# Kernel tuning notes

Hardware: AMD Instinct MI355X
Metric: run time of the kernel (lower is better)

Reference implementation:

```python
import jax, jax.numpy as jnp
import numpy as np

_CODESZ = 8
_INT_MAP = (2 ** np.arange(_CODESZ))[::-1].astype(np.int32)  # [128,64,...,1], MSB = dim 0

_NORM12 = np.array([
    [3,1,1,1,3,3,3,3],[1,3,1,1,3,3,3,3],[1,1,3,1,3,3,3,3],[1,1,1,3,3,3,3,3],
    [3,3,3,1,3,3,1,1],[3,3,3,1,3,1,3,1],[3,3,3,1,1,3,3,1],[3,3,3,1,3,1,1,3],
    [3,3,3,1,1,3,1,3],[3,3,3,1,1,1,3,3],[3,3,1,3,3,3,1,1],[3,3,1,3,3,1,3,1],
    [3,3,1,3,1,3,3,1],[3,3,1,3,3,1,1,3],[3,3,1,3,1,3,1,3],[3,3,1,3,1,1,3,3],
    [3,1,3,3,3,3,1,1],[3,1,3,3,3,1,3,1],[3,1,3,3,1,3,3,1],[3,1,3,3,3,1,1,3],
    [3,1,3,3,1,3,1,3],[1,3,3,3,1,1,3,3],[1,3,3,3,3,3,1,1],[1,3,3,3,3,1,3,1],
    [1,3,3,3,1,3,3,1],[1,3,3,3,3,1,1,3],[1,3,3,3,1,3,1,3],[1,3,3,3,1,1,3,3],
    [3,3,1,1,3,3,3,1]], dtype=np.float32) / 2.0


def _build_codebook():
    # abs grid: nonneg half-integer vectors with norm^2 <= 10 == abs of even-sum D8+1/2 shell
    vals = np.array([0.5, 1.5, 2.5], np.float32)  # 3.5^2 > 10, so components <= 2.5
    pts = np.stack(np.meshgrid(*([vals] * _CODESZ), indexing='ij'), -1).reshape(-1, _CODESZ)
    pts = pts[(pts * pts).sum(-1) <= 10.0]                      # 227 rows
    pts = pts[np.lexsort(pts[:, ::-1].T)]                       # torch.unique(dim=0) order
    absg = np.concatenate([pts, _NORM12], 0)                    # [256, 8]

    bits = ((np.arange(256)[:, None] & _INT_MAP[None, :]) > 0).astype(np.int32)  # [256,8]
    pop = bits.sum(-1)
    even_ids = np.where(pop % 2 == 0)[0]                        # 128 even-parity masks
    odd_ids = np.where(pop % 2 == 1)[0]
    signs_even = (1 - 2 * bits[even_ids]).astype(np.float32)    # [128,8]
    signs_odd = (1 - 2 * bits[odd_ids]).astype(np.float32)
    # valid sign parity per abs entry so flipped point has even coordinate sum
    g_even = (absg.sum(-1) % 2.0) == 0.0
    S = np.where(g_even[:, None, None], signs_even[None], signs_odd[None])  # [256,128,8]
    P = (S * absg[:, None, :]).reshape(-1, _CODESZ)             # [32768,8] shell points
    # full grid = [P + 1/4 ; P - 1/4]  (grid[:half] - 1/4 == P, as the module assumes)

    # grid_part: canonical representatives (dims 1: have <=1 negative, min >= -0.5)
    sel = ((P[:, 1:] < 0).sum(-1) <= 1) & (P[:, 1:].min(-1) >= -0.5)
    grid_part = P[sel]                                          # [G,8]
    grid_part_norm = (grid_part * grid_part).sum(-1)            # [G]

    # iterate_mask: even-parity flips x grid_part -> index into grid
    flips = (1 - 2 * bits[even_ids]).astype(np.float32)         # [128,8]
    idx_map = np.zeros(256, np.int32)
    idx_map[even_ids] = np.arange(128, dtype=np.int32)
    gridH = P + 0.25                                            # first half of grid
    gridHn = (gridH * gridH).sum(-1)
    allcombo_idx = np.zeros((128, len(grid_part)), np.int32)
    for i in range(128):  # small fixed loop over sign masks, as in the original
        sc = 2.0 * ((flips[i] * grid_part) @ gridH.T) - gridHn
        allcombo_idx[i] = np.argmax(sc, -1).astype(np.int32)
    # _E8P_GRID_IDX taken as identity permutation -> grid_idx_map = arange - 2^15 (int16)
    grid_idx_map = (np.arange(2 ** 16) - 2 ** 15).astype(np.int16)
    return grid_part, grid_part_norm, allcombo_idx, idx_map, grid_idx_map


def setup_inputs() -> dict:
    key = jax.random.key(0)
    N = 131072
    grid_part, gpn, aci, imap, gim = _build_codebook()
    X = jax.random.normal(key, (N, _CODESZ), dtype=jnp.float32)
    return {
        'X': X,
        'grid_part': jnp.asarray(grid_part),
        'grid_part_norm': jnp.asarray(gpn),
        'allcombo_idx': jnp.asarray(aci),
        'idx_map': jnp.asarray(imap),
        'int_map': jnp.asarray(_INT_MAP),
        'grid_idx_map': jnp.asarray(gim),
    }


def reference(X, grid_part, grid_part_norm, allcombo_idx, idx_map, int_map, grid_idx_map):
    def fast_quantize_part(Y):
        neg = Y < 0                                              # [N,8]
        odd = (neg.sum(-1) % 2) == 1                             # [N] odd # of negatives
        Ya = jnp.abs(Y)
        Ya = Ya.at[:, 0].set(jnp.where(odd, -Ya[:, 0], Ya[:, 0]))
        mask = jnp.where(neg, -1.0, 1.0).astype(Y.dtype)
        mask = mask.at[:, 0].set(jnp.where(odd, -mask[:, 0], mask[:, 0]))
        # nearest codeword: argmax(2 Y.g - |g|^2)  == argmin |Y - g|^2
        q = jnp.argmax(2.0 * (Ya @ grid_part.T) - grid_part_norm, axis=-1)  # [N]
        vals = grid_part[q] * mask
        mint = (((1.0 - mask) * 0.5).astype(jnp.int32) * int_map).sum(-1)   # bit-pack signs
        real_idx = allcombo_idx[idx_map[mint], q]
        err = jnp.sqrt(((Y - vals) ** 2).sum(-1))
        return vals, real_idx, err

    HALF = 2 ** 15
    pv, pi, pe = fast_quantize_part(X + 0.25)
    mv, mi, me = fast_quantize_part(X - 0.25)
    which = pe < me
    final_vals = jnp.where(which[:, None], pv - 0.25, mv + 0.25)
    final_idxs = grid_idx_map[jnp.where(which, pi + HALF, mi)]
    return final_vals, final_idxs
```

## Files before the change

### kernel.cpp

```cpp
#include <hip/hip_runtime.h>
#include <hip/hip_bf16.h>

typedef __attribute__((ext_vector_type(8)))  short bf16x8;
typedef __attribute__((ext_vector_type(16))) float f32x16;

#define TPB 256
#define SCORE_MARGIN 1e-3f
#define ERR_MARGIN   1e-3f

static __device__ __forceinline__ unsigned short bf16_rne(float v) {
    union { __hip_bfloat16 h; unsigned short u; } cv;
    cv.h = __float2bfloat16(v);
    return cv.u;
}
static __device__ __forceinline__ float bfhi(unsigned u) { return __uint_as_float(u << 16); }
static __device__ __forceinline__ float bflo(unsigned u) { return __uint_as_float(u & 0xffff0000u); }

__global__ __launch_bounds__(TPB, 4) void e8p_fused(
    const float* __restrict__ X,
    const float* __restrict__ grid_part,
    const float* __restrict__ grid_part_norm,
    const int*   __restrict__ allcombo_idx,
    const int*   __restrict__ idx_map,
    float* __restrict__ out,
    int N, int G, int T)
{
    extern __shared__ __align__(16) unsigned char smem[];
    const int T32 = T * 32;
    unsigned char* ldsG = smem;
    unsigned short* ldsN = (unsigned short*)(smem + (size_t)T32 * 16);

    const int tid = threadIdx.x;

    for (int c = tid; c < T32; c += TPB) {
        uint4 gv; float nv;
        if (c < G) {
            const float4 g0 = *(const float4*)(grid_part + (size_t)c * 8);
            const float4 g1 = *(const float4*)(grid_part + (size_t)c * 8 + 4);
            gv.x = (unsigned)bf16_rne(g0.x) | ((unsigned)bf16_rne(g0.y) << 16);
            gv.y = (unsigned)bf16_rne(g0.z) | ((unsigned)bf16_rne(g0.w) << 16);
            gv.z = (unsigned)bf16_rne(g1.x) | ((unsigned)bf16_rne(g1.y) << 16);
            gv.w = (unsigned)bf16_rne(g1.z) | ((unsigned)bf16_rne(g1.w) << 16);
            nv = -0.5f * grid_part_norm[c];
        } else {
            gv.x = gv.y = gv.z = gv.w = 0u;
            nv = -30000.0f;
        }
        *(uint4*)(ldsG + (size_t)c * 16) = gv;
        const int t = c >> 5, w = c & 31;
        const int hh = (w >> 2) & 1;
        const int rr = (w & 3) + 4 * (w >> 3);
        ldsN[t * 32 + hh * 16 + rr] = bf16_rne(nv);
    }
    __syncthreads();

    const int lane = tid & 63;
    const int h    = lane >> 5;
    const int col  = lane & 31;
    const int wave = blockIdx.x * (TPB / 64) + (tid >> 6);

    const int li     = col >> 1;
    const int branch = col & 1;
    const int irow   = wave * 16 + li;
    const int iload  = (irow < N) ? irow : 0;

    float x[8];
    {
        const float4 a = *(const float4*)(X + (size_t)iload * 8);
        const float4 b = *(const float4*)(X + (size_t)iload * 8 + 4);
        x[0]=a.x; x[1]=a.y; x[2]=a.z; x[3]=a.w;
        x[4]=b.x; x[5]=b.y; x[6]=b.z; x[7]=b.w;
    }

    float ya[8]; int neg = 0;
    const float sh = branch ? -0.25f : 0.25f;
#pragma unroll
    for (int j = 0; j < 8; ++j) {
        const float yj = x[j] + sh;
        if (yj < 0.0f) neg |= (1 << (7 - j));
        ya[j] = fabsf(yj);
    }
    int mint = neg;
    if (__popc(neg) & 1) { ya[0] = -ya[0]; mint ^= 128; }

    bf16x8 bfrag;
#pragma unroll
    for (int j = 0; j < 8; ++j) {
        const unsigned short hi = bf16_rne(ya[j]);
        const unsigned short lo = bf16_rne(ya[j] - bfhi((unsigned)hi));
        bfrag[j] = (short)(h ? lo : hi);
    }

    float best[4], sec[4]; int qt[4];
#pragma unroll
    for (int g = 0; g < 4; ++g) { best[g] = -1e30f; sec[g] = -1e30f; qt[g] = 0; }

    const unsigned aoff = (unsigned)col * 16u;
    const unsigned char* nbase = (const unsigned char*)ldsN + h * 32;

    bf16x8 afragN = *(const bf16x8*)(ldsG + aoff);
    uint4 n0N = *(const uint4*)(nbase);
    uint4 n1N = *(const uint4*)(nbase + 16);

    for (int t = 0; t < T; ++t) {
        const bf16x8 afrag = afragN;
        const uint4 n0 = n0N, n1 = n1N;
        const int tn = (t + 1 < T) ? (t + 1) : t;
        afragN = *(const bf16x8*)(ldsG + (size_t)tn * 512 + aoff);
        n0N = *(const uint4*)(nbase + (size_t)tn * 64);
        n1N = *(const uint4*)(nbase + (size_t)tn * 64 + 16);

        f32x16 acc;
        acc[0]=bfhi(n0.x);  acc[1]=bflo(n0.x);  acc[2]=bfhi(n0.y);  acc[3]=bflo(n0.y);
        acc[4]=bfhi(n0.z);  acc[5]=bflo(n0.z);  acc[6]=bfhi(n0.w);  acc[7]=bflo(n0.w);
        acc[8]=bfhi(n1.x);  acc[9]=bflo(n1.x);  acc[10]=bfhi(n1.y); acc[11]=bflo(n1.y);
        acc[12]=bfhi(n1.z); acc[13]=bflo(n1.z); acc[14]=bfhi(n1.w); acc[15]=bflo(n1.w);
        acc = __builtin_amdgcn_mfma_f32_32x32x16_bf16(afrag, bfrag, acc, 0, 0, 0);

#pragma unroll
        for (int g = 0; g < 4; ++g) {
            const float m = fmaxf(fmaxf(acc[4*g], acc[4*g+1]),
                                  fmaxf(acc[4*g+2], acc[4*g+3]));
            const bool gt = m > best[g];
            sec[g]  = __builtin_amdgcn_fmed3f(m, best[g], sec[g]);
            best[g] = fmaxf(best[g], m);
            qt[g]   = gt ? t : qt[g];
        }
    }

    float bb = best[0], ss = sec[0];
    int   ib = (qt[0] << 5) + 4 * h;
#pragma unroll
    for (int g = 1; g < 4; ++g) {
        const int ibg = (qt[g] << 5) + 8 * g + 4 * h;
        const float br = best[g];
        ss = fmaxf(fmaxf(ss, sec[g]), fminf(bb, br));
        const bool take = (br > bb) || ((br == bb) && (ibg < ib));
        bb = fmaxf(bb, br);
        ib = take ? ibg : ib;
    }
    {
        const float ob = __shfl_xor(bb, 32, 64);
        const float os = __shfl_xor(ss, 32, 64);
        const int   oi = __shfl_xor(ib, 32, 64);
        ss = fmaxf(fmaxf(ss, os), fminf(bb, ob));
        const bool take = (ob > bb) || ((ob == bb) && (oi < ib));
        bb = fmaxf(bb, ob);
        ib = take ? oi : ib;
    }

    float hiF[8], loF[8];
#pragma unroll
    for (int j = 0; j < 8; ++j) {
        hiF[j] = bfhi((unsigned)bf16_rne(ya[j]));
        loF[j] = ya[j] - hiF[j];
    }
    const int tW   = ib >> 5;
    const int base = ib & 31;
    float sm = -1e30f, sec4 = -1e30f; int km = 0;
#pragma unroll
    for (int k = 0; k < 4; ++k) {
        const int w  = base + k;
        const uint4 gv = *(const uint4*)(ldsG + ((size_t)tW * 32 + w) * 16);
        const int hn = (w >> 2) & 1;
        const int rn = (w & 3) + 4 * (w >> 3);
        const float nv = bfhi((unsigned)ldsN[tW * 32 + hn * 16 + rn]);
        float g0 = bfhi(gv.x), g1 = bflo(gv.x), g2 = bfhi(gv.y), g3 = bflo(gv.y);
        float g4 = bfhi(gv.z), g5 = bflo(gv.z), g6 = bfhi(gv.w), g7 = bflo(gv.w);
        float s = nv;
        s = fmaf(hiF[0], g0, s); s = fmaf(hiF[1], g1, s);
        s = fmaf(hiF[2], g2, s); s = fmaf(hiF[3], g3, s);
        s = fmaf(hiF[4], g4, s); s = fmaf(hiF[5], g5, s);
        s = fmaf(hiF[6], g6, s); s = fmaf(hiF[7], g7, s);
        s = fmaf(loF[0], g0, s); s = fmaf(loF[1], g1, s);
        s = fmaf(loF[2], g2, s); s = fmaf(loF[3], g3, s);
        s = fmaf(loF[4], g4, s); s = fmaf(loF[5], g5, s);
        s = fmaf(loF[6], g6, s); s = fmaf(loF[7], g7, s);
        const bool gt = s > sm;
        sec4 = __builtin_amdgcn_fmed3f(s, sm, sec4);
        sm   = fmaxf(sm, s);
        km   = gt ? k : km;
    }
    const int  qfin   = tW * 32 + base + km;
    const int  closeB = ((sm - sec4) < SCORE_MARGIN) | ((bb - ss) < SCORE_MARGIN);

    const int qO     = __shfl_xor(qfin, 1, 64);
    const int closeO = __shfl_xor(closeB, 1, 64);
    const int mintO  = __shfl_xor(mint, 1, 64);

    const bool doEpi = (h == 0) && (branch == 0) && (irow < N);
    bool close = false;
    if (doEpi) {
        const int qP = qfin, qM = qO;
        const float* gp_ = grid_part + (size_t)qP * 8;
        const float* gm_ = grid_part + (size_t)qM * 8;
        float vp[8], vm[8];
        float ep2 = 0.0f, em2 = 0.0f;
        bool coin = true;
#pragma unroll
        for (int j = 0; j < 8; ++j) {
            const float maskp = ((mint  >> (7 - j)) & 1) ? -1.0f : 1.0f;
            const float maskm = ((mintO >> (7 - j)) & 1) ? -1.0f : 1.0f;
            vp[j] = gp_[j] * maskp;
            vm[j] = gm_[j] * maskm;
            coin = coin && ((vp[j] - 0.25f) == (vm[j] + 0.25f));
            const float dpj = (x[j] + 0.25f) - vp[j];
            const float dmj = (x[j] - 0.25f) - vm[j];
            ep2 = fmaf(dpj, dpj, ep2);
            em2 = fmaf(dmj, dmj, em2);
        }
        close = closeB | closeO | (!coin && (fabsf(ep2 - em2) < ERR_MARGIN));
        if (!close) {
            const bool which = coin ? false : (ep2 < em2);
            const int rowp = idx_map[mint];
            const int rowm = idx_map[mintO];
            const int pi = allcombo_idx[(size_t)rowp * G + qP];
            const int mi = allcombo_idx[(size_t)rowm * G + qM];
            const float idxval = which ? (float)pi : (float)(mi - 32768);
            float* vout = out + (size_t)irow * 8;
#pragma unroll
            for (int j = 0; j < 8; ++j)
                vout[j] = which ? (vp[j] - 0.25f) : (vm[j] + 0.25f);
            out[(size_t)N * 8 + irow] = idxval;
        }
    }

    unsigned long long mb = __ballot(doEpi && close);
    while (mb) {
        const int b = (int)__ffsll(mb) - 1;
        mb &= (mb - 1);
        const int liF = b >> 1;
        const int iF  = wave * 16 + liF;
        float xf[8];
#pragma unroll
        for (int j = 0; j < 8; ++j) xf[j] = __shfl(x[j], b, 64);

        double yapF[8], yamF[8];
        int negp = 0, negm = 0;
#pragma unroll
        for (int j = 0; j < 8; ++j) {
            const double xd = (double)xf[j];
            const double ypd = xd + 0.25;
            const double ymd = xd - 0.25;
            if (ypd < 0.0) negp |= (1 << (7 - j));
            if (ymd < 0.0) negm |= (1 << (7 - j));
            yapF[j] = fabs(ypd);
            yamF[j] = fabs(ymd);
        }
        int mintpF = negp, mintmF = negm;
        if (__popc(negp) & 1) { yapF[0] = -yapF[0]; mintpF ^= 128; }
        if (__popc(negm) & 1) { yamF[0] = -yamF[0]; mintmF ^= 128; }

        double bestpF = -1e300, bestmF = -1e300;
        int qpF = 0x7fffffff, qmF = 0x7fffffff;
        for (int j = lane; j < G; j += 64) {
            const float4 g0 = *(const float4*)(grid_part + (size_t)j * 8);
            const float4 g1 = *(const float4*)(grid_part + (size_t)j * 8 + 4);
            const double n = (double)grid_part_norm[j];
            const double t0 = (double)g0.x, t1 = (double)g0.y,
                         t2 = (double)g0.z, t3 = (double)g0.w,
                         t4 = (double)g1.x, t5 = (double)g1.y,
                         t6 = (double)g1.z, t7 = (double)g1.w;
            double dp, dm;
            dp = yapF[0] * t0;           dm = yamF[0] * t0;
            dp = fma(yapF[1], t1, dp);   dm = fma(yamF[1], t1, dm);
            dp = fma(yapF[2], t2, dp);   dm = fma(yamF[2], t2, dm);
            dp = fma(yapF[3], t3, dp);   dm = fma(yamF[3], t3, dm);
            dp = fma(yapF[4], t4, dp);   dm = fma(yamF[4], t4, dm);
            dp = fma(yapF[5], t5, dp);   dm = fma(yamF[5], t5, dm);
            dp = fma(yapF[6], t6, dp);   dm = fma(yamF[6], t6, dm);
            dp = fma(yapF[7], t7, dp);   dm = fma(yamF[7], t7, dm);
            const double sp = 2.0 * dp - n;
            const double sm2 = 2.0 * dm - n;
            if (sp > bestpF) { bestpF = sp; qpF = j; }
            if (sm2 > bestmF) { bestmF = sm2; qmF = j; }
        }
#pragma unroll
        for (int off = 32; off > 0; off >>= 1) {
            double ob = __shfl_xor(bestpF, off, 64);
            int    oq = __shfl_xor(qpF, off, 64);
            if (ob > bestpF || (ob == bestpF && oq < qpF)) { bestpF = ob; qpF = oq; }
            ob = __shfl_xor(bestmF, off, 64);
            oq = __shfl_xor(qmF, off, 64);
            if (ob > bestmF || (ob == bestmF && oq < qmF)) { bestmF = ob; qmF = oq; }
        }
        if (lane == 0) {
            const float* gp_ = grid_part + (size_t)qpF * 8;
            const float* gm_ = grid_part + (size_t)qmF * 8;
            double vp[8], vm[8];
            double ep2 = 0.0, em2 = 0.0;
#pragma unroll
            for (int j = 0; j < 8; ++j) {
                const double maskp = ((mintpF >> (7 - j)) & 1) ? -1.0 : 1.0;
                const double maskm = ((mintmF >> (7 - j)) & 1) ? -1.0 : 1.0;
                vp[j] = (double)gp_[j] * maskp;
                vm[j] = (double)gm_[j] * maskm;
                const double xd = (double)xf[j];
                const double dpj = (xd + 0.25) - vp[j];
                const double dmj = (xd - 0.25) - vm[j];
                ep2 += dpj * dpj;
                em2 += dmj * dmj;
            }
            const double ep = sqrt(ep2), em = sqrt(em2);
            const bool which = ep < em;
            const int rowp = idx_map[mintpF];
            const int rowm = idx_map[mintmF];
            const int pi = allcombo_idx[(size_t)rowp * G + qpF];
            const int mi = allcombo_idx[(size_t)rowm * G + qmF];
            const float idxval = which ? (float)pi : (float)(mi - 32768);
            float* vout = out + (size_t)iF * 8;
#pragma unroll
            for (int j = 0; j < 8; ++j) {
                const double v = which ? (vp[j] - 0.25) : (vm[j] + 0.25);
                vout[j] = (float)v;
            }
            out[(size_t)N * 8 + iF] = idxval;
        }
    }
}

extern "C" void kernel_launch(void* const* d_in, const int* in_sizes, int n_in,
                              void* d_out, int out_size, void* d_ws, size_t ws_size,
                              hipStream_t stream) {
    const float* X    = (const float*)d_in[0];
    const float* gp   = (const float*)d_in[1];
    const float* gn   = (const float*)d_in[2];
    const int*   aci  = (const int*)d_in[3];
    const int*   imap = (const int*)d_in[4];

    const int N = in_sizes[0] / 8;
    const int G = in_sizes[1] / 8;
    const int T = (G + 31) / 32;
    const int blocks = (N + 63) / 64;
    const size_t shmem = (size_t)T * 512 + (size_t)T * 64;

    hipLaunchKernelGGL(e8p_fused, dim3(blocks), dim3(TPB), shmem, stream,
                       X, gp, gn, aci, imap, (float*)d_out, N, G, T);
}
```

Baseline: 138.5 us.

## Bucket codewords by norm so MFMA accumulates from zero and adds per-group bias

Codewords are sorted in shared memory into buckets by squared norm, and each bucket is padded to a multiple of four. Every 4-row group the MFMA produces then shares one norm bias. The MFMA can start from a zero accumulator, and the bias becomes one scalar add per group after the max, replacing 16 bf16 unpacks per tile. This assumes norms fall into six even integer values (2..12), which holds for this codebook. It adds an atomic counting sort per block, a remap table back to original indices, and padding rows that are flagged as close so they are handled exactly.

New measurement: 140.4 us. No clear change (+1.4%).

```diff
diff --git a/kernel.cpp b/kernel.cpp
--- a/kernel.cpp
+++ b/kernel.cpp
@@ -28,29 +28,58 @@
     extern __shared__ __align__(16) unsigned char smem[];
     const int T32 = T * 32;
     unsigned char* ldsG = smem;
-    unsigned short* ldsN = (unsigned short*)(smem + (size_t)T32 * 16);
+    float*         ldsNg = (float*)(smem + (size_t)T32 * 16);
+    int*           ldsI  = (int*)((unsigned char*)ldsNg + (size_t)T * 32);
+
+    __shared__ int cnt[6];
+    __shared__ int cur[6];
 
     const int tid = threadIdx.x;
 
     for (int c = tid; c < T32; c += TPB) {
-        uint4 gv; float nv;
-        if (c < G) {
-            const float4 g0 = *(const float4*)(grid_part + (size_t)c * 8);
-            const float4 g1 = *(const float4*)(grid_part + (size_t)c * 8 + 4);
-            gv.x = (unsigned)bf16_rne(g0.x) | ((unsigned)bf16_rne(g0.y) << 16);
-            gv.y = (unsigned)bf16_rne(g0.z) | ((unsigned)bf16_rne(g0.w) << 16);
-            gv.z = (unsigned)bf16_rne(g1.x) | ((unsigned)bf16_rne(g1.y) << 16);
-            gv.w = (unsigned)bf16_rne(g1.z) | ((unsigned)bf16_rne(g1.w) << 16);
-            nv = -0.5f * grid_part_norm[c];
-        } else {
-            gv.x = gv.y = gv.z = gv.w = 0u;
-            nv = -30000.0f;
-        }
-        *(uint4*)(ldsG + (size_t)c * 16) = gv;
-        const int t = c >> 5, w = c & 31;
-        const int hh = (w >> 2) & 1;
-        const int rr = (w & 3) + 4 * (w >> 3);
-        ldsN[t * 32 + hh * 16 + rr] = bf16_rne(nv);
+        uint4 z; z.x = z.y = z.z = z.w = 0u;
+        *(uint4*)(ldsG + (size_t)c * 16) = z;
+        ldsI[c] = -1;
+    }
+    for (int c = tid; c < T * 8; c += TPB) ldsNg[c] = -30000.0f;
+    if (tid < 6) cnt[tid] = 0;
+    if (tid >= 6 && tid < 12) cur[tid - 6] = 0;
+    __syncthreads();
+
+    for (int c = tid; c < G; c += TPB) {
+        const int k = (__float2int_rn(grid_part_norm[c]) >> 1) - 1;
+        atomicAdd(&cnt[k], 1);
+    }
+    __syncthreads();
+
+    int offs[6];
+    {
+        int o = 0;
+#pragma unroll
+        for (int k = 0; k < 6; ++k) { offs[k] = o; o += (cnt[k] + 3) & ~3; }
+    }
+
+    for (int c = tid; c < G; c += TPB) {
+        const int k = (__float2int_rn(grid_part_norm[c]) >> 1) - 1;
+        const int pos = offs[k] + atomicAdd(&cur[k], 1);
+        const float4 g0 = *(const float4*)(grid_part + (size_t)c * 8);
+        const float4 g1 = *(const float4*)(grid_part + (size_t)c * 8 + 4);
+        uint4 gv;
+        gv.x = (unsigned)bf16_rne(g0.x) | ((unsigned)bf16_rne(g0.y) << 16);
+        gv.y = (unsigned)bf16_rne(g0.z) | ((unsigned)bf16_rne(g0.w) << 16);
+        gv.z = (unsigned)bf16_rne(g1.x) | ((unsigned)bf16_rne(g1.y) << 16);
+        gv.w = (unsigned)bf16_rne(g1.z) | ((unsigned)bf16_rne(g1.w) << 16);
+        *(uint4*)(ldsG + (size_t)pos * 16) = gv;
+        ldsI[pos] = c;
+    }
+    for (int gi = tid; gi < T * 8; gi += TPB) {
+        const int t = gi >> 3, hh = (gi >> 2) & 1, gg = gi & 3;
+        const int p4 = t * 32 + 8 * gg + 4 * hh;
+        float v = -30000.0f;
+#pragma unroll
+        for (int k = 0; k < 6; ++k)
+            if (p4 >= offs[k] && p4 < offs[k] + cnt[k]) v = -(float)(k + 1);
+        ldsNg[gi] = v;
     }
     __syncthreads();
 
@@ -96,34 +125,29 @@
     for (int g = 0; g < 4; ++g) { best[g] = -1e30f; sec[g] = -1e30f; qt[g] = 0; }
 
     const unsigned aoff = (unsigned)col * 16u;
-    const unsigned char* nbase = (const unsigned char*)ldsN + h * 32;
+    const float* ngbase = ldsNg + h * 4;
 
     bf16x8 afragN = *(const bf16x8*)(ldsG + aoff);
-    uint4 n0N = *(const uint4*)(nbase);
-    uint4 n1N = *(const uint4*)(nbase + 16);
-
+    float4 ngvN   = *(const float4*)(ngbase);
+
+    const f32x16 czero = {0,0,0,0,0,0,0,0,0,0,0,0,0,0,0,0};
     for (int t = 0; t < T; ++t) {
         const bf16x8 afrag = afragN;
-        const uint4 n0 = n0N, n1 = n1N;
+        const float4 ngv   = ngvN;
         const int tn = (t + 1 < T) ? (t + 1) : t;
         afragN = *(const bf16x8*)(ldsG + (size_t)tn * 512 + aoff);
-        n0N = *(const uint4*)(nbase + (size_t)tn * 64);
-        n1N = *(const uint4*)(nbase + (size_t)tn * 64 + 16);
-
-        f32x16 acc;
-        acc[0]=bfhi(n0.x);  acc[1]=bflo(n0.x);  acc[2]=bfhi(n0.y);  acc[3]=bflo(n0.y);
-        acc[4]=bfhi(n0.z);  acc[5]=bflo(n0.z);  acc[6]=bfhi(n0.w);  acc[7]=bflo(n0.w);
-        acc[8]=bfhi(n1.x);  acc[9]=bflo(n1.x);  acc[10]=bfhi(n1.y); acc[11]=bflo(n1.y);
-        acc[12]=bfhi(n1.z); acc[13]=bflo(n1.z); acc[14]=bfhi(n1.w); acc[15]=bflo(n1.w);
-        acc = __builtin_amdgcn_mfma_f32_32x32x16_bf16(afrag, bfrag, acc, 0, 0, 0);
-
+        ngvN   = *(const float4*)(ngbase + (size_t)tn * 8);
+
+        const f32x16 acc = __builtin_amdgcn_mfma_f32_32x32x16_bf16(afrag, bfrag, czero, 0, 0, 0);
+        const float ng[4] = {ngv.x, ngv.y, ngv.z, ngv.w};
 #pragma unroll
         for (int g = 0; g < 4; ++g) {
             const float m = fmaxf(fmaxf(acc[4*g], acc[4*g+1]),
                                   fmaxf(acc[4*g+2], acc[4*g+3]));
-            const bool gt = m > best[g];
-            sec[g]  = __builtin_amdgcn_fmed3f(m, best[g], sec[g]);
-            best[g] = fmaxf(best[g], m);
+            const float s = m + ng[g];
+            const bool gt = s > best[g];
+            sec[g]  = __builtin_amdgcn_fmed3f(s, best[g], sec[g]);
+            best[g] = fmaxf(best[g], s);
             qt[g]   = gt ? t : qt[g];
         }
     }
@@ -157,17 +181,14 @@
     }
     const int tW   = ib >> 5;
     const int base = ib & 31;
+    const float ngW = ldsNg[tW * 8 + ((base >> 2) & 1) * 4 + (base >> 3)];
     float sm = -1e30f, sec4 = -1e30f; int km = 0;
 #pragma unroll
     for (int k = 0; k < 4; ++k) {
-        const int w  = base + k;
-        const uint4 gv = *(const uint4*)(ldsG + ((size_t)tW * 32 + w) * 16);
-        const int hn = (w >> 2) & 1;
-        const int rn = (w & 3) + 4 * (w >> 3);
-        const float nv = bfhi((unsigned)ldsN[tW * 32 + hn * 16 + rn]);
-        float g0 = bfhi(gv.x), g1 = bflo(gv.x), g2 = bfhi(gv.y), g3 = bflo(gv.y);
-        float g4 = bfhi(gv.z), g5 = bflo(gv.z), g6 = bfhi(gv.w), g7 = bflo(gv.w);
-        float s = nv;
+        const uint4 gv = *(const uint4*)(ldsG + ((size_t)tW * 32 + base + k) * 16);
+        const float g0 = bfhi(gv.x), g1 = bflo(gv.x), g2 = bfhi(gv.y), g3 = bflo(gv.y);
+        const float g4 = bfhi(gv.z), g5 = bflo(gv.z), g6 = bfhi(gv.w), g7 = bflo(gv.w);
+        float s = ngW;
         s = fmaf(hiF[0], g0, s); s = fmaf(hiF[1], g1, s);
         s = fmaf(hiF[2], g2, s); s = fmaf(hiF[3], g3, s);
         s = fmaf(hiF[4], g4, s); s = fmaf(hiF[5], g5, s);
@@ -181,17 +202,19 @@
         sm   = fmaxf(sm, s);
         km   = gt ? k : km;
     }
-    const int  qfin   = tW * 32 + base + km;
-    const int  closeB = ((sm - sec4) < SCORE_MARGIN) | ((bb - ss) < SCORE_MARGIN);
-
-    const int qO     = __shfl_xor(qfin, 1, 64);
+    int orig = ldsI[tW * 32 + base + km];
+    int closeB = ((sm - sec4) < SCORE_MARGIN) | ((bb - ss) < SCORE_MARGIN) |
+                 (orig < 0);
+    if (orig < 0) orig = 0;
+
+    const int qO     = __shfl_xor(orig, 1, 64);
     const int closeO = __shfl_xor(closeB, 1, 64);
     const int mintO  = __shfl_xor(mint, 1, 64);
 
     const bool doEpi = (h == 0) && (branch == 0) && (irow < N);
     bool close = false;
     if (doEpi) {
-        const int qP = qfin, qM = qO;
+        const int qP = orig, qM = qO;
         const float* gp_ = grid_part + (size_t)qP * 8;
         const float* gm_ = grid_part + (size_t)qM * 8;
         float vp[8], vm[8];
@@ -330,9 +353,9 @@
 
     const int N = in_sizes[0] / 8;
     const int G = in_sizes[1] / 8;
-    const int T = (G + 31) / 32;
+    const int T = (G + 18 + 31) / 32;
     const int blocks = (N + 63) / 64;
-    const size_t shmem = (size_t)T * 512 + (size_t)T * 64;
+    const size_t shmem = (size_t)T * 32 * 16 + (size_t)T * 32 + (size_t)T * 32 * 4;
 
     hipLaunchKernelGGL(e8p_fused, dim3(blocks), dim3(TPB), shmem, stream,
                        X, gp, gn, aci, imap, (float*)d_out, N, G, T);
```

## Process two codeword tiles per iteration and tighten near-tie fallback margins

Applied to the files above, without the earlier changes.

The main scan loop now issues two independent MFMAs per iteration over a pair of 32-codeword tiles, with T padded to an even count, so the matrix unit has more independent work in flight and loop overhead is halved. The fixed score and error margins that route rows to the exact fallback path are replaced by a tighter, input-magnitude-scaled score margin and a smaller error margin, so fewer rows take the slow recheck. Candidate indices past G are clamped to zero. The risk is extra register pressure from the doubled accumulators and a chance of misclassifying near-ties if the tighter margins are too small for the bf16 rounding error.

New measurement: 126.6 us. 1.09x faster.

```diff
diff --git a/kernel.cpp b/kernel.cpp
--- a/kernel.cpp
+++ b/kernel.cpp
@@ -5,8 +5,7 @@
 typedef __attribute__((ext_vector_type(16))) float f32x16;
 
 #define TPB 256
-#define SCORE_MARGIN 1e-3f
-#define ERR_MARGIN   1e-3f
+#define ERR_MARGIN   1e-4f
 
 static __device__ __forceinline__ unsigned short bf16_rne(float v) {
     union { __hip_bfloat16 h; unsigned short u; } cv;
@@ -26,11 +25,11 @@
     int N, int G, int T)
 {
     extern __shared__ __align__(16) unsigned char smem[];
+    unsigned char*  ldsCW = smem;
+    unsigned short* ldsNG = (unsigned short*)(smem + (size_t)T * 512);
+
+    const int tid = threadIdx.x;
     const int T32 = T * 32;
-    unsigned char* ldsG = smem;
-    unsigned short* ldsN = (unsigned short*)(smem + (size_t)T32 * 16);
-
-    const int tid = threadIdx.x;
 
     for (int c = tid; c < T32; c += TPB) {
         uint4 gv; float nv;
@@ -46,11 +45,11 @@
             gv.x = gv.y = gv.z = gv.w = 0u;
             nv = -30000.0f;
         }
-        *(uint4*)(ldsG + (size_t)c * 16) = gv;
+        *(uint4*)(ldsCW + (size_t)c * 16) = gv;
         const int t = c >> 5, w = c & 31;
         const int hh = (w >> 2) & 1;
         const int rr = (w & 3) + 4 * (w >> 3);
-        ldsN[t * 32 + hh * 16 + rr] = bf16_rne(nv);
+        ldsNG[t * 32 + hh * 16 + rr] = bf16_rne(nv);
     }
     __syncthreads();
 
@@ -73,15 +72,19 @@
     }
 
     float ya[8]; int neg = 0;
+    float sya = 0.0f;
     const float sh = branch ? -0.25f : 0.25f;
 #pragma unroll
     for (int j = 0; j < 8; ++j) {
         const float yj = x[j] + sh;
         if (yj < 0.0f) neg |= (1 << (7 - j));
         ya[j] = fabsf(yj);
+        sya += fabsf(yj);
     }
     int mint = neg;
     if (__popc(neg) & 1) { ya[0] = -ya[0]; mint ^= 128; }
+
+    const float SM = fmaf(5e-5f, sya, 2e-5f);
 
     bf16x8 bfrag;
 #pragma unroll
@@ -95,36 +98,59 @@
 #pragma unroll
     for (int g = 0; g < 4; ++g) { best[g] = -1e30f; sec[g] = -1e30f; qt[g] = 0; }
 
-    const unsigned aoff = (unsigned)col * 16u;
-    const unsigned char* nbase = (const unsigned char*)ldsN + h * 32;
-
-    bf16x8 afragN = *(const bf16x8*)(ldsG + aoff);
-    uint4 n0N = *(const uint4*)(nbase);
-    uint4 n1N = *(const uint4*)(nbase + 16);
-
-    for (int t = 0; t < T; ++t) {
-        const bf16x8 afrag = afragN;
-        const uint4 n0 = n0N, n1 = n1N;
-        const int tn = (t + 1 < T) ? (t + 1) : t;
-        afragN = *(const bf16x8*)(ldsG + (size_t)tn * 512 + aoff);
-        n0N = *(const uint4*)(nbase + (size_t)tn * 64);
-        n1N = *(const uint4*)(nbase + (size_t)tn * 64 + 16);
-
-        f32x16 acc;
-        acc[0]=bfhi(n0.x);  acc[1]=bflo(n0.x);  acc[2]=bfhi(n0.y);  acc[3]=bflo(n0.y);
-        acc[4]=bfhi(n0.z);  acc[5]=bflo(n0.z);  acc[6]=bfhi(n0.w);  acc[7]=bflo(n0.w);
-        acc[8]=bfhi(n1.x);  acc[9]=bflo(n1.x);  acc[10]=bfhi(n1.y); acc[11]=bflo(n1.y);
-        acc[12]=bfhi(n1.z); acc[13]=bflo(n1.z); acc[14]=bfhi(n1.w); acc[15]=bflo(n1.w);
-        acc = __builtin_amdgcn_mfma_f32_32x32x16_bf16(afrag, bfrag, acc, 0, 0, 0);
+    const unsigned char* aptr = ldsCW + (unsigned)col * 16u;
+    const unsigned char* nptr = (const unsigned char*)ldsNG + h * 32;
+
+    const int P = T >> 1;
+    bf16x8 a0N = *(const bf16x8*)(aptr);
+    bf16x8 a1N = *(const bf16x8*)(aptr + 512);
+    uint4  m0N = *(const uint4*)(nptr);
+    uint4  m1N = *(const uint4*)(nptr + 16);
+    uint4  m2N = *(const uint4*)(nptr + 64);
+    uint4  m3N = *(const uint4*)(nptr + 80);
+
+    for (int p = 0; p < P; ++p) {
+        const bf16x8 af0 = a0N, af1 = a1N;
+        const uint4 n0 = m0N, n1 = m1N, n2 = m2N, n3 = m3N;
+        const int pn = (p + 1 < P) ? (p + 1) : p;
+        a0N = *(const bf16x8*)(aptr + (size_t)pn * 1024);
+        a1N = *(const bf16x8*)(aptr + (size_t)pn * 1024 + 512);
+        m0N = *(const uint4*)(nptr + (size_t)pn * 128);
+        m1N = *(const uint4*)(nptr + (size_t)pn * 128 + 16);
+        m2N = *(const uint4*)(nptr + (size_t)pn * 128 + 64);
+        m3N = *(const uint4*)(nptr + (size_t)pn * 128 + 80);
+
+        f32x16 acc0;
+        acc0[0]=bfhi(n0.x);  acc0[1]=bflo(n0.x);  acc0[2]=bfhi(n0.y);  acc0[3]=bflo(n0.y);
+        acc0[4]=bfhi(n0.z);  acc0[5]=bflo(n0.z);  acc0[6]=bfhi(n0.w);  acc0[7]=bflo(n0.w);
+        acc0[8]=bfhi(n1.x);  acc0[9]=bflo(n1.x);  acc0[10]=bfhi(n1.y); acc0[11]=bflo(n1.y);
+        acc0[12]=bfhi(n1.z); acc0[13]=bflo(n1.z); acc0[14]=bfhi(n1.w); acc0[15]=bflo(n1.w);
+        f32x16 acc1;
+        acc1[0]=bfhi(n2.x);  acc1[1]=bflo(n2.x);  acc1[2]=bfhi(n2.y);  acc1[3]=bflo(n2.y);
+        acc1[4]=bfhi(n2.z);  acc1[5]=bflo(n2.z);  acc1[6]=bfhi(n2.w);  acc1[7]=bflo(n2.w);
+        acc1[8]=bfhi(n3.x);  acc1[9]=bflo(n3.x);  acc1[10]=bfhi(n3.y); acc1[11]=bflo(n3.y);
+        acc1[12]=bfhi(n3.z); acc1[13]=bflo(n3.z); acc1[14]=bfhi(n3.w); acc1[15]=bflo(n3.w);
+
+        acc0 = __builtin_amdgcn_mfma_f32_32x32x16_bf16(af0, bfrag, acc0, 0, 0, 0);
+        acc1 = __builtin_amdgcn_mfma_f32_32x32x16_bf16(af1, bfrag, acc1, 0, 0, 0);
 
 #pragma unroll
         for (int g = 0; g < 4; ++g) {
-            const float m = fmaxf(fmaxf(acc[4*g], acc[4*g+1]),
-                                  fmaxf(acc[4*g+2], acc[4*g+3]));
+            const float m = fmaxf(fmaxf(fmaxf(acc0[4*g], acc0[4*g+1]), acc0[4*g+2]),
+                                  acc0[4*g+3]);
             const bool gt = m > best[g];
             sec[g]  = __builtin_amdgcn_fmed3f(m, best[g], sec[g]);
             best[g] = fmaxf(best[g], m);
-            qt[g]   = gt ? t : qt[g];
+            qt[g]   = gt ? (2 * p) : qt[g];
+        }
+#pragma unroll
+        for (int g = 0; g < 4; ++g) {
+            const float m = fmaxf(fmaxf(fmaxf(acc1[4*g], acc1[4*g+1]), acc1[4*g+2]),
+                                  acc1[4*g+3]);
+            const bool gt = m > best[g];
+            sec[g]  = __builtin_amdgcn_fmed3f(m, best[g], sec[g]);
+            best[g] = fmaxf(best[g], m);
+            qt[g]   = gt ? (2 * p + 1) : qt[g];
         }
     }
 
@@ -157,17 +183,16 @@
     }
     const int tW   = ib >> 5;
     const int base = ib & 31;
+    const int hW   = (base >> 2) & 1;
+    const int rW0  = 4 * (base >> 3);
+    const unsigned short* nW = ldsNG + tW * 32 + hW * 16 + rW0;
     float sm = -1e30f, sec4 = -1e30f; int km = 0;
 #pragma unroll
     for (int k = 0; k < 4; ++k) {
-        const int w  = base + k;
-        const uint4 gv = *(const uint4*)(ldsG + ((size_t)tW * 32 + w) * 16);
-        const int hn = (w >> 2) & 1;
-        const int rn = (w & 3) + 4 * (w >> 3);
-        const float nv = bfhi((unsigned)ldsN[tW * 32 + hn * 16 + rn]);
-        float g0 = bfhi(gv.x), g1 = bflo(gv.x), g2 = bfhi(gv.y), g3 = bflo(gv.y);
-        float g4 = bfhi(gv.z), g5 = bflo(gv.z), g6 = bfhi(gv.w), g7 = bflo(gv.w);
-        float s = nv;
+        const uint4 gv = *(const uint4*)(ldsCW + ((size_t)tW * 32 + base + k) * 16);
+        const float g0 = bfhi(gv.x), g1 = bflo(gv.x), g2 = bfhi(gv.y), g3 = bflo(gv.y);
+        const float g4 = bfhi(gv.z), g5 = bflo(gv.z), g6 = bfhi(gv.w), g7 = bflo(gv.w);
+        float s = bfhi((unsigned)nW[k]);
         s = fmaf(hiF[0], g0, s); s = fmaf(hiF[1], g1, s);
         s = fmaf(hiF[2], g2, s); s = fmaf(hiF[3], g3, s);
         s = fmaf(hiF[4], g4, s); s = fmaf(hiF[5], g5, s);
@@ -181,17 +206,18 @@
         sm   = fmaxf(sm, s);
         km   = gt ? k : km;
     }
-    const int  qfin   = tW * 32 + base + km;
-    const int  closeB = ((sm - sec4) < SCORE_MARGIN) | ((bb - ss) < SCORE_MARGIN);
-
-    const int qO     = __shfl_xor(qfin, 1, 64);
+    int orig = tW * 32 + base + km;
+    const int closeB = ((sm - sec4) < SM) | ((bb - ss) < SM);
+    if (orig >= G) orig = 0;
+
+    const int qO     = __shfl_xor(orig, 1, 64);
     const int closeO = __shfl_xor(closeB, 1, 64);
     const int mintO  = __shfl_xor(mint, 1, 64);
 
     const bool doEpi = (h == 0) && (branch == 0) && (irow < N);
     bool close = false;
     if (doEpi) {
-        const int qP = qfin, qM = qO;
+        const int qP = orig, qM = qO;
         const float* gp_ = grid_part + (size_t)qP * 8;
         const float* gm_ = grid_part + (size_t)qM * 8;
         float vp[8], vm[8];
@@ -330,7 +356,8 @@
 
     const int N = in_sizes[0] / 8;
     const int G = in_sizes[1] / 8;
-    const int T = (G + 31) / 32;
+    int T = (G + 31) / 32;
+    T += (T & 1);
     const int blocks = (N + 63) / 64;
     const size_t shmem = (size_t)T * 512 + (size_t)T * 64;
 
```
